# Optimization experiments

Hardware: AMD Instinct MI355X
Metric: run time of the kernel (lower is better)

## Reference

```python
import jax, jax.numpy as jnp
import numpy as np

EPS = 1e-9
NUM_HEADS = 16
D = 1024      # input_dim == hidden_dim
B, S = 2, 2048


def layer_norm(x, scale, shift):
    mu = x.mean(axis=-1, keepdims=True)
    # torch std is unbiased (ddof=1); eps added to std, not variance
    std = jnp.std(x, axis=-1, ddof=1, keepdims=True)
    return scale * (x - mu) / (std + EPS) + shift


def setup_inputs() -> dict:
    key = jax.random.key(0)
    ks = jax.random.split(key, 18)
    d, h = D, D
    w = lambda k, sh: jax.random.normal(k, sh, dtype=jnp.float32) * 0.02
    return {
        "inputs": jax.random.normal(ks[0], (B, S, d), dtype=jnp.float32),
        "ln1_scale": jax.random.normal(ks[1], (d,), dtype=jnp.float32),
        "ln1_shift": jax.random.normal(ks[2], (d,), dtype=jnp.float32),
        "Wq": w(ks[3], (d, h)), "bq": jnp.zeros((h,), jnp.float32),
        "Wk": w(ks[4], (d, h)), "bk": jnp.zeros((h,), jnp.float32),
        "Wv": w(ks[5], (d, h)), "bv": jnp.zeros((h,), jnp.float32),
        "Wo": w(ks[6], (h, d)), "bo": jnp.zeros((d,), jnp.float32),
        "W1": w(ks[7], (d, 4 * d)), "b1": jnp.zeros((4 * d,), jnp.float32),
        "W2": w(ks[8], (4 * d, d)), "b2": jnp.zeros((d,), jnp.float32),
        "ln2_scale": jax.random.normal(ks[9], (d,), dtype=jnp.float32),
        "ln2_shift": jax.random.normal(ks[10], (d,), dtype=jnp.float32),
    }


def mhsa(x, Wq, bq, Wk, bk, Wv, bv, Wo, bo):
    b, s, d = x.shape
    nh, dh = NUM_HEADS, D // NUM_HEADS
    q = (x @ Wq + bq).reshape(b, s, nh, dh).transpose(0, 2, 1, 3)  # b h s d
    k = (x @ Wk + bk).reshape(b, s, nh, dh).transpose(0, 2, 1, 3)
    v = (x @ Wv + bv).reshape(b, s, nh, dh).transpose(0, 2, 1, 3)
    scores = jnp.einsum("bhqd,bhkd->bhqk", q, k) / jnp.sqrt(jnp.float32(dh))
    causal = jnp.triu(jnp.ones((s, s), dtype=bool), k=1)  # mask above diagonal
    scores = jnp.where(causal, -jnp.inf, scores)
    p = jax.nn.softmax(scores, axis=-1)
    p = jnp.where(jnp.isnan(p), 0.0, p)  # NaN-fill as in original
    out = jnp.einsum("bhqk,bhkd->bhqd", p, v)
    out = out.transpose(0, 2, 1, 3).reshape(b, s, nh * dh)
    return out @ Wo + bo


def reference(inputs, ln1_scale, ln1_shift, Wq, bq, Wk, bk, Wv, bv, Wo, bo,
              W1, b1, W2, b2, ln2_scale, ln2_shift):
    o1 = layer_norm(inputs, ln1_scale, ln1_shift)
    o1 = mhsa(o1, Wq, bq, Wk, bk, Wv, bv, Wo, bo) + inputs
    o2 = layer_norm(o1, ln2_scale, ln2_shift)
    # NOTE: original adds the residual from the *normalized* tensor, not o1
    ffn = jax.nn.relu(o2 @ W1 + b1) @ W2 + b2
    return ffn + o2
```

## Files before the change

### kernel.cpp

```cpp
#include <hip/hip_runtime.h>
#include <hip/hip_bf16.h>
#include <math.h>

#define BB 2
#define SS 2048
#define DD 1024
#define HH 16
#define DH 64
#define NROW (BB*SS)
#define FFN (4*DD)

typedef __attribute__((ext_vector_type(8))) __bf16 bf16x8;
typedef __attribute__((ext_vector_type(4))) float f32x4;

__device__ __forceinline__ ushort f2b(float f) {
    union { float f; uint32_t u; } x; x.f = f;
    uint32_t r = x.u + 0x7FFF + ((x.u >> 16) & 1);
    return (ushort)(r >> 16);
}
__device__ __forceinline__ float b2f(ushort u) {
    union { uint32_t u; float f; } x; x.u = (uint32_t)u << 16;
    return x.f;
}

__global__ __launch_bounds__(256)
void ln_kernel(const float* __restrict__ x, const float* __restrict__ scale,
               const float* __restrict__ shift, ushort* __restrict__ y) {
    int row = blockIdx.x;
    const float* xr = x + (size_t)row * DD;
    ushort* yr = y + (size_t)row * DD;
    int t = threadIdx.x;
    float v[4];
    float s = 0.f, ss = 0.f;
#pragma unroll
    for (int i = 0; i < 4; ++i) {
        v[i] = xr[t + 256 * i];
        s += v[i];
        ss += v[i] * v[i];
    }
#pragma unroll
    for (int off = 32; off; off >>= 1) {
        s  += __shfl_xor(s, off);
        ss += __shfl_xor(ss, off);
    }
    __shared__ float red[8];
    int w = t >> 6;
    if ((t & 63) == 0) { red[w] = s; red[w + 4] = ss; }
    __syncthreads();
    float st  = red[0] + red[1] + red[2] + red[3];
    float sst = red[4] + red[5] + red[6] + red[7];
    float mu = st * (1.f / DD);
    float var = (sst - DD * mu * mu) * (1.f / (DD - 1));
    var = fmaxf(var, 0.f);
    float inv = 1.f / (sqrtf(var) + 1e-9f);
#pragma unroll
    for (int i = 0; i < 4; ++i) {
        int c = t + 256 * i;
        yr[c] = f2b(scale[c] * (v[i] - mu) * inv + shift[c]);
    }
}

__global__ __launch_bounds__(256)
void ln_res_kernel(const ushort* __restrict__ xa, const float* __restrict__ xb,
                   const float* __restrict__ scale, const float* __restrict__ shift,
                   ushort* __restrict__ yb) {
    int row = blockIdx.x;
    const ushort* ar = xa + (size_t)row * DD;
    const float* br = xb + (size_t)row * DD;
    ushort* ybr = yb + (size_t)row * DD;
    int t = threadIdx.x;
    float v[4];
    float s = 0.f, ss = 0.f;
#pragma unroll
    for (int i = 0; i < 4; ++i) {
        int c = t + 256 * i;
        v[i] = b2f(ar[c]) + br[c];
        s += v[i];
        ss += v[i] * v[i];
    }
#pragma unroll
    for (int off = 32; off; off >>= 1) {
        s  += __shfl_xor(s, off);
        ss += __shfl_xor(ss, off);
    }
    __shared__ float red[8];
    int w = t >> 6;
    if ((t & 63) == 0) { red[w] = s; red[w + 4] = ss; }
    __syncthreads();
    float st  = red[0] + red[1] + red[2] + red[3];
    float sst = red[4] + red[5] + red[6] + red[7];
    float mu = st * (1.f / DD);
    float var = (sst - DD * mu * mu) * (1.f / (DD - 1));
    var = fmaxf(var, 0.f);
    float inv = 1.f / (sqrtf(var) + 1e-9f);
#pragma unroll
    for (int i = 0; i < 4; ++i) {
        int c = t + 256 * i;
        ybr[c] = f2b(scale[c] * (v[i] - mu) * inv + shift[c]);
    }
}

__global__ __launch_bounds__(256)
void transpose_bf16_kernel(const float* __restrict__ W, ushort* __restrict__ Wt,
                           int K, int N) {
    __shared__ ushort tile[32][33];
    int tx = threadIdx.x & 31;
    int ty = threadIdx.x >> 5;
    int n0 = blockIdx.x * 32;
    int k0 = blockIdx.y * 32;
#pragma unroll
    for (int i = 0; i < 32; i += 8)
        tile[ty + i][tx] = f2b(W[(size_t)(k0 + ty + i) * N + n0 + tx]);
    __syncthreads();
#pragma unroll
    for (int i = 0; i < 32; i += 8)
        Wt[(size_t)(n0 + ty + i) * K + k0 + tx] = tile[tx][ty + i];
}

__global__ __launch_bounds__(256)
void reduce_wo_kernel(const float* __restrict__ p0, const float* __restrict__ p1,
                      const float* __restrict__ bias, ushort* __restrict__ yb) {
    int i = (blockIdx.x * 256 + threadIdx.x) * 4;
    float4 a = *reinterpret_cast<const float4*>(p0 + i);
    float4 b = *reinterpret_cast<const float4*>(p1 + i);
    int c = i & (DD - 1);
    float4 bs = *reinterpret_cast<const float4*>(bias + c);
    ushort4 o;
    o.x = f2b(a.x + b.x + bs.x);
    o.y = f2b(a.y + b.y + bs.y);
    o.z = f2b(a.z + b.z + bs.z);
    o.w = f2b(a.w + b.w + bs.w);
    *reinterpret_cast<ushort4*>(yb + i) = o;
}

__global__ __launch_bounds__(256)
void reduce_ffn2_kernel(const float* __restrict__ p0, const float* __restrict__ p1,
                        const float* __restrict__ bias, const ushort* __restrict__ res,
                        float* __restrict__ out) {
    int i = (blockIdx.x * 256 + threadIdx.x) * 4;
    float4 a = *reinterpret_cast<const float4*>(p0 + i);
    float4 b = *reinterpret_cast<const float4*>(p1 + i);
    ushort4 r = *reinterpret_cast<const ushort4*>(res + i);
    int c = i & (DD - 1);
    float4 bs = *reinterpret_cast<const float4*>(bias + c);
    float4 o;
    o.x = a.x + b.x + bs.x + b2f(r.x);
    o.y = a.y + b.y + bs.y + b2f(r.y);
    o.z = a.z + b.z + bs.z + b2f(r.z);
    o.w = a.w + b.w + bs.w + b2f(r.w);
    *reinterpret_cast<float4*>(out + i) = o;
}

#define GBM 128
#define GBN 128
#define GBK 32

template <int MODE, bool BF16_OUT, int DEPTH>
__global__ __launch_bounds__(512)
void gemm_bf16_kernel(const ushort* __restrict__ A, const ushort* __restrict__ Wt,
                      const float* __restrict__ bias, const ushort* __restrict__ addsrc,
                      void* __restrict__ Cout, int M, int N, int K, int lda,
                      const float* __restrict__ bias2, const float* __restrict__ bias3,
                      void* __restrict__ out2, void* __restrict__ out3) {
    __shared__ ushort As[DEPTH][GBM * GBK];
    __shared__ ushort Bs[DEPTH][GBN * GBK];

    int tid = threadIdx.x;
    int lane = tid & 63;
    int wid = tid >> 6;
    int wr = wid >> 2, wc = wid & 3;

    int gx = gridDim.x;
    int nwg = gx * gridDim.y;
    int orig = blockIdx.y * gx + blockIdx.x;
    int q8 = nwg >> 3;
    int swz = (orig & 7) * q8 + (orig >> 3);
    int bx = swz % gx, by = swz / gx;

    int brow = by * GBM;
    int bcol = bx * GBN;
    size_t koff = (size_t)blockIdx.z * K;

    int lrow = lane & 15;
    int kgrp = lane >> 4;

    f32x4 acc[4][2] = {};

    int srow = tid >> 2;
    int sgran = (tid & 3) ^ ((srow >> 1) & 3);

    auto stage = [&](int buf, int k0) {
        const char* ga = (const char*)A +
            ((size_t)(brow + srow) * lda + koff + k0) * 2 + sgran * 16;
        __builtin_amdgcn_global_load_lds(
            (const __attribute__((address_space(1))) uint32_t*)ga,
            (__attribute__((address_space(3))) uint32_t*)(&As[buf][0] + (wid * 16) * GBK),
            16, 0, 0);
        const char* gb = (const char*)Wt +
            ((size_t)(bcol + srow) * lda + koff + k0) * 2 + sgran * 16;
        __builtin_amdgcn_global_load_lds(
            (const __attribute__((address_space(1))) uint32_t*)gb,
            (__attribute__((address_space(3))) uint32_t*)(&Bs[buf][0] + (wid * 16) * GBK),
            16, 0, 0);
    };

    int nk = K / GBK;
    constexpr int PRE = DEPTH - 1;
#pragma unroll
    for (int s = 0; s < PRE; ++s)
        if (s < nk) stage(s, s * GBK);

    int cur = 0, stg = PRE;
    for (int t = 0; t < nk; ++t) {
        __builtin_amdgcn_sched_barrier(0);
        int rem = nk - 1 - t;
        if constexpr (DEPTH == 5) {
            if (rem >= 3)      asm volatile("s_waitcnt vmcnt(6)" ::: "memory");
            else if (rem == 2) asm volatile("s_waitcnt vmcnt(4)" ::: "memory");
            else if (rem == 1) asm volatile("s_waitcnt vmcnt(2)" ::: "memory");
            else               asm volatile("s_waitcnt vmcnt(0)" ::: "memory");
        } else {
            if (rem >= 1)      asm volatile("s_waitcnt vmcnt(2)" ::: "memory");
            else               asm volatile("s_waitcnt vmcnt(0)" ::: "memory");
        }
        asm volatile("s_barrier" ::: "memory");
        if (t + PRE < nk) stage(stg, (t + PRE) * GBK);

        bf16x8 afrag[4], bfrag[2];
#pragma unroll
        for (int mi = 0; mi < 4; ++mi) {
            int row = wr * 64 + mi * 16 + lrow;
            int gran = kgrp ^ ((row >> 1) & 3);
            afrag[mi] = *(const bf16x8*)((const char*)&As[cur][0] + row * 64 + gran * 16);
        }
#pragma unroll
        for (int ni = 0; ni < 2; ++ni) {
            int row = wc * 32 + ni * 16 + lrow;
            int gran = kgrp ^ ((row >> 1) & 3);
            bfrag[ni] = *(const bf16x8*)((const char*)&Bs[cur][0] + row * 64 + gran * 16);
        }
#pragma unroll
        for (int mi = 0; mi < 4; ++mi)
#pragma unroll
            for (int ni = 0; ni < 2; ++ni)
                acc[mi][ni] = __builtin_amdgcn_mfma_f32_16x16x32_bf16(
                    afrag[mi], bfrag[ni], acc[mi][ni], 0, 0, 0);

        cur = (cur == DEPTH - 1) ? 0 : cur + 1;
        stg = (stg == DEPTH - 1) ? 0 : stg + 1;
    }

    if (MODE == 3) {
        int which = bcol >> 10;
        const float* bs = which == 0 ? bias : (which == 1 ? bias2 : bias3);
#pragma unroll
        for (int ni = 0; ni < 2; ++ni) {
            int col = bcol + wc * 32 + ni * 16 + lrow;
            int lcol = col & 1023;
            float bsv = bs[lcol];
#pragma unroll
            for (int mi = 0; mi < 4; ++mi) {
                f32x4 a = acc[mi][ni];
#pragma unroll
                for (int j = 0; j < 4; ++j) {
                    int row = brow + wr * 64 + mi * 16 + kgrp * 4 + j;
                    float val = a[j] + bsv;
                    if (which == 2) {
                        size_t idx = (size_t)(row >> 11) * ((size_t)DD * SS)
                                   + (size_t)lcol * SS + (row & (SS - 1));
                        ((ushort*)out3)[idx] = f2b(val);
                    } else {
                        ushort* dst = which == 0 ? (ushort*)Cout : (ushort*)out2;
                        dst[(size_t)row * DD + lcol] = f2b(val);
                    }
                }
            }
        }
        return;
    }

    if (MODE == 4) {
        float* dst = (float*)Cout + (size_t)blockIdx.z * ((size_t)M * N);
#pragma unroll
        for (int ni = 0; ni < 2; ++ni) {
            int col = bcol + wc * 32 + ni * 16 + lrow;
#pragma unroll
            for (int mi = 0; mi < 4; ++mi) {
                f32x4 a = acc[mi][ni];
#pragma unroll
                for (int j = 0; j < 4; ++j) {
                    int row = brow + wr * 64 + mi * 16 + kgrp * 4 + j;
                    dst[(size_t)row * N + col] = a[j];
                }
            }
        }
        return;
    }

#pragma unroll
    for (int ni = 0; ni < 2; ++ni) {
        int col = bcol + wc * 32 + ni * 16 + lrow;
        float bsv = bias[col];
#pragma unroll
        for (int mi = 0; mi < 4; ++mi) {
            f32x4 a = acc[mi][ni];
#pragma unroll
            for (int j = 0; j < 4; ++j) {
                int row = brow + wr * 64 + mi * 16 + kgrp * 4 + j;
                float val = a[j] + bsv;
                if (MODE == 1) val = fmaxf(val, 0.f);
                if (BF16_OUT)
                    ((ushort*)Cout)[(size_t)row * N + col] = f2b(val);
                else
                    ((float*)Cout)[(size_t)row * N + col] = val;
            }
        }
    }
}

__global__ __launch_bounds__(256)
void attn_mfma_kernel(const ushort* __restrict__ Qg, const ushort* __restrict__ Kg,
                      const ushort* __restrict__ Vtg, ushort* __restrict__ Og) {
    __shared__ ushort Qs[64 * 64];
    __shared__ ushort Ks[2][64 * 64];
    __shared__ ushort Vs[2][64 * 64];

    int tid = threadIdx.x;
    int lane = tid & 63;
    int wid = tid >> 6;
    int bh = blockIdx.x;
    int b = bh >> 4, h = bh & 15;
    int q0 = ((int)gridDim.y - 1 - (int)blockIdx.y) * 64;

    const ushort* Qbase = Qg + ((size_t)(b * SS + q0)) * DD + h * DH;
    const ushort* Kbase = Kg + ((size_t)(b * SS)) * DD + h * DH;
    const ushort* Vbase = Vtg + (size_t)bh * DH * SS;

    int r0 = wid * 16;
    int rr0 = r0 + (lane >> 3);
    int g0 = lane & 7;
    int g = lane >> 4;
    int lr = lane & 15;

    auto stageKV = [&](int buf, int k0) {
#pragma unroll
        for (int i = 0; i < 2; ++i) {
            int rr = rr0 + i * 8;
            int gg = g0 ^ (rr & 7);
            const ushort* srck = Kbase + (size_t)(k0 + rr) * DD + gg * 8;
            __builtin_amdgcn_global_load_lds(
                (const __attribute__((address_space(1))) uint32_t*)srck,
                (__attribute__((address_space(3))) uint32_t*)(&Ks[buf][0] + (r0 + i * 8) * 64),
                16, 0, 0);
            const ushort* srcv = Vbase + (size_t)rr * SS + k0 + gg * 8;
            __builtin_amdgcn_global_load_lds(
                (const __attribute__((address_space(1))) uint32_t*)srcv,
                (__attribute__((address_space(3))) uint32_t*)(&Vs[buf][0] + (r0 + i * 8) * 64),
                16, 0, 0);
        }
    };

    int nt = q0 / 64 + 1;

    {
#pragma unroll
        for (int i = 0; i < 2; ++i) {
            int rr = rr0 + i * 8;
            int gg = g0 ^ (rr & 7);
            const ushort* src = Qbase + (size_t)rr * DD + gg * 8;
            __builtin_amdgcn_global_load_lds(
                (const __attribute__((address_space(1))) uint32_t*)src,
                (__attribute__((address_space(3))) uint32_t*)(Qs + (r0 + i * 8) * 64),
                16, 0, 0);
        }
    }
    stageKV(0, 0);
    asm volatile("s_waitcnt vmcnt(4)" ::: "memory");

    bf16x8 aq[2];
    {
        int r = wid * 16 + lr;
#pragma unroll
        for (int ks = 0; ks < 2; ++ks) {
            int lg = ks * 4 + g;
            aq[ks] = *(const bf16x8*)((const char*)Qs + r * 128 + ((lg ^ (r & 7)) << 4));
        }
    }
    ushort* Ps = Qs;

    f32x4 oacc[4] = {};
    float m = -INFINITY, l = 0.f;
    int qa = q0 + wid * 16 + lr;

    int cur = 0;
    for (int t = 0; t < nt; ++t) {
        __builtin_amdgcn_sched_barrier(0);
        asm volatile("s_waitcnt vmcnt(0)" ::: "memory");
        asm volatile("s_barrier" ::: "memory");
        if (t + 1 < nt) stageKV(cur ^ 1, (t + 1) * 64);
        int k0 = t * 64;

        f32x4 sacc[4] = {};
        __builtin_amdgcn_s_setprio(1);
#pragma unroll
        for (int ni = 0; ni < 4; ++ni) {
            int r = ni * 16 + lr;
#pragma unroll
            for (int ks = 0; ks < 2; ++ks) {
                int lg = ks * 4 + g;
                bf16x8 bk = *(const bf16x8*)((const char*)&Ks[cur][0] + r * 128 + ((lg ^ (r & 7)) << 4));
                sacc[ni] = __builtin_amdgcn_mfma_f32_16x16x32_bf16(bk, aq[ks], sacc[ni], 0, 0, 0);
            }
        }
        __builtin_amdgcn_s_setprio(0);

        float sc[4][4];
#pragma unroll
        for (int ni = 0; ni < 4; ++ni)
#pragma unroll
            for (int j = 0; j < 4; ++j)
                sc[ni][j] = sacc[ni][j] * 0.125f;
        if (k0 == q0) {
#pragma unroll
            for (int ni = 0; ni < 4; ++ni) {
#pragma unroll
                for (int j = 0; j < 4; ++j) {
                    int key = q0 + ni * 16 + g * 4 + j;
                    if (key > qa) sc[ni][j] = -INFINITY;
                }
            }
        }

        float mx = sc[0][0];
#pragma unroll
        for (int ni = 0; ni < 4; ++ni)
#pragma unroll
            for (int j = 0; j < 4; ++j) mx = fmaxf(mx, sc[ni][j]);
        mx = fmaxf(mx, __shfl_xor(mx, 16));
        mx = fmaxf(mx, __shfl_xor(mx, 32));
        float mn = fmaxf(m, mx);
        float corr = __expf(m - mn);
        m = mn;
        float p[4][4];
        float rs = 0.f;
#pragma unroll
        for (int ni = 0; ni < 4; ++ni)
#pragma unroll
            for (int j = 0; j < 4; ++j) { p[ni][j] = __expf(sc[ni][j] - mn); rs += p[ni][j]; }
        rs += __shfl_xor(rs, 16);
        rs += __shfl_xor(rs, 32);
        l = l * corr + rs;

        float cj[4];
#pragma unroll
        for (int j = 0; j < 4; ++j)
            cj[j] = __shfl(corr, (lane & 48) | (g * 4 + j));
#pragma unroll
        for (int ni = 0; ni < 4; ++ni)
#pragma unroll
            for (int j = 0; j < 4; ++j) oacc[ni][j] *= cj[j];

        {
            int row = wid * 16 + lr;
#pragma unroll
            for (int ni = 0; ni < 4; ++ni) {
                ushort4 w4;
                w4.x = f2b(p[ni][0]); w4.y = f2b(p[ni][1]);
                w4.z = f2b(p[ni][2]); w4.w = f2b(p[ni][3]);
                int gran = (ni * 2 + (g >> 1)) ^ (row & 7);
                *(ushort4*)((char*)Ps + row * 128 + (gran << 4) + (g & 1) * 8) = w4;
            }
        }
        asm volatile("s_waitcnt lgkmcnt(0)" ::: "memory");

        bf16x8 ap[2];
        {
            int r = wid * 16 + lr;
#pragma unroll
            for (int ks = 0; ks < 2; ++ks) {
                int lg = ks * 4 + g;
                ap[ks] = *(const bf16x8*)((const char*)Ps + r * 128 + ((lg ^ (r & 7)) << 4));
            }
        }
        __builtin_amdgcn_s_setprio(1);
#pragma unroll
        for (int ni = 0; ni < 4; ++ni) {
            int r = ni * 16 + lr;
#pragma unroll
            for (int ks = 0; ks < 2; ++ks) {
                int lg = ks * 4 + g;
                bf16x8 bv = *(const bf16x8*)((const char*)&Vs[cur][0] + r * 128 + ((lg ^ (r & 7)) << 4));
                oacc[ni] = __builtin_amdgcn_mfma_f32_16x16x32_bf16(ap[ks], bv, oacc[ni], 0, 0, 0);
            }
        }
        __builtin_amdgcn_s_setprio(0);
        cur ^= 1;
    }

#pragma unroll
    for (int j = 0; j < 4; ++j) {
        float lj = __shfl(l, (lane & 48) | (g * 4 + j));
        float inv = 1.f / lj;
        int gr = q0 + wid * 16 + g * 4 + j;
#pragma unroll
        for (int ni = 0; ni < 4; ++ni) {
            int d = ni * 16 + lr;
            Og[((size_t)(b * SS + gr)) * DD + h * DH + d] = f2b(oacc[ni][j] * inv);
        }
    }
}

extern "C" void kernel_launch(void* const* d_in, const int* in_sizes, int n_in,
                              void* d_out, int out_size, void* d_ws, size_t ws_size,
                              hipStream_t stream) {
    const float* inputs    = (const float*)d_in[0];
    const float* ln1_scale = (const float*)d_in[1];
    const float* ln1_shift = (const float*)d_in[2];
    const float* Wq = (const float*)d_in[3];
    const float* bq = (const float*)d_in[4];
    const float* Wk = (const float*)d_in[5];
    const float* bk = (const float*)d_in[6];
    const float* Wv = (const float*)d_in[7];
    const float* bv = (const float*)d_in[8];
    const float* Wo = (const float*)d_in[9];
    const float* bo = (const float*)d_in[10];
    const float* W1 = (const float*)d_in[11];
    const float* b1 = (const float*)d_in[12];
    const float* W2 = (const float*)d_in[13];
    const float* b2 = (const float*)d_in[14];
    const float* ln2_scale = (const float*)d_in[15];
    const float* ln2_shift = (const float*)d_in[16];
    float* out = (float*)d_out;

    const size_t MB = 1024 * 1024;
    char* w = (char*)d_ws;
    ushort* q_b   = (ushort*)(w + 0 * MB);
    ushort* k_b   = (ushort*)(w + 8 * MB);
    ushort* vt_b  = (ushort*)(w + 16 * MB);
    ushort* att_b = (ushort*)(w + 24 * MB);
    float*  pw    = (float*)(w + 32 * MB);
    ushort* proj_b= (ushort*)(w + 0 * MB);
    ushort* o2_b  = (ushort*)(w + 8 * MB);
    float*  pf    = (float*)(w + 16 * MB);
    ushort* h1_b  = (ushort*)(w + 64 * MB);
    ushort* wq_t  = (ushort*)(w + 96 * MB);
    ushort* wk_t  = (ushort*)(w + 98 * MB);
    ushort* wv_t  = (ushort*)(w + 100 * MB);
    ushort* wo_t  = (ushort*)(w + 102 * MB);
    ushort* w1_t  = (ushort*)(w + 104 * MB);
    ushort* w2_t  = (ushort*)(w + 112 * MB);
    ushort* xn_b  = (ushort*)(w + 120 * MB);

    transpose_bf16_kernel<<<dim3(DD / 32, DD / 32), 256, 0, stream>>>(Wq, wq_t, DD, DD);
    transpose_bf16_kernel<<<dim3(DD / 32, DD / 32), 256, 0, stream>>>(Wk, wk_t, DD, DD);
    transpose_bf16_kernel<<<dim3(DD / 32, DD / 32), 256, 0, stream>>>(Wv, wv_t, DD, DD);
    transpose_bf16_kernel<<<dim3(DD / 32, DD / 32), 256, 0, stream>>>(Wo, wo_t, DD, DD);
    transpose_bf16_kernel<<<dim3(FFN / 32, DD / 32), 256, 0, stream>>>(W1, w1_t, DD, FFN);
    transpose_bf16_kernel<<<dim3(DD / 32, FFN / 32), 256, 0, stream>>>(W2, w2_t, FFN, DD);

    ln_kernel<<<NROW, 256, 0, stream>>>(inputs, ln1_scale, ln1_shift, xn_b);

    dim3 gqkv(3 * DD / GBN, NROW / GBM, 1);
    gemm_bf16_kernel<3, true, 3><<<gqkv, 512, 0, stream>>>(
        xn_b, wq_t, bq, nullptr, q_b, NROW, 3 * DD, DD, DD, bk, bv, k_b, vt_b);

    dim3 ga(BB * HH, SS / 64);
    attn_mfma_kernel<<<ga, 256, 0, stream>>>(q_b, k_b, vt_b, att_b);

    dim3 g1z(DD / GBN, NROW / GBM, 2);
    gemm_bf16_kernel<4, false, 5><<<g1z, 512, 0, stream>>>(
        att_b, wo_t, nullptr, nullptr, pw, NROW, DD, DD / 2, DD, nullptr, nullptr, nullptr, nullptr);
    reduce_wo_kernel<<<(NROW * DD / 4) / 256, 256, 0, stream>>>(
        pw, pw + (size_t)NROW * DD, bo, proj_b);

    ln_res_kernel<<<NROW, 256, 0, stream>>>(proj_b, inputs, ln2_scale, ln2_shift, o2_b);

    dim3 g2(FFN / GBN, NROW / GBM, 1);
    gemm_bf16_kernel<1, true, 3><<<g2, 512, 0, stream>>>(
        o2_b, w1_t, b1, nullptr, h1_b, NROW, FFN, DD, DD, nullptr, nullptr, nullptr, nullptr);

    gemm_bf16_kernel<4, false, 5><<<g1z, 512, 0, stream>>>(
        h1_b, w2_t, nullptr, nullptr, pf, NROW, DD, FFN / 2, FFN, nullptr, nullptr, nullptr, nullptr);
    reduce_ffn2_kernel<<<(NROW * DD / 4) / 256, 256, 0, stream>>>(
        pf, pf + (size_t)NROW * DD, b2, o2_b, out);
}
```

Baseline: 257.0 us.

## Fold softmax scale into Q, use exp2 with lazy rescaling and remapped tile order

Pre-multiplies Q by log2(e)/sqrt(dh) in the projection epilogue so attention can use native exp2 without a per-score multiply. Adds FA4-style lazy rescaling that skips the output correction unless the running max grows by more than a threshold, and switches P conversion to native bf16 casts. Also changes the query-tile order across blockIdx.y to a serpentine pattern instead of strict reverse. The lazy rescaling lets p values exceed 1, up to about 2^11, which raises bf16 rounding error and overflow risk. The new tile order may also hurt load balance across the causal triangle.

```diff
diff --git a/kernel.cpp b/kernel.cpp
--- a/kernel.cpp
+++ b/kernel.cpp
@@ -11,7 +11,10 @@
 #define FFN (4*DD)
 
 typedef __attribute__((ext_vector_type(8))) __bf16 bf16x8;
+typedef __attribute__((ext_vector_type(4))) __bf16 bf16x4;
 typedef __attribute__((ext_vector_type(4))) float f32x4;
+
+#define QSCALE 0.18033688011112042f
 
 __device__ __forceinline__ ushort f2b(float f) {
     union { float f; uint32_t u; } x; x.f = f;
@@ -269,9 +272,10 @@
                         size_t idx = (size_t)(row >> 11) * ((size_t)DD * SS)
                                    + (size_t)lcol * SS + (row & (SS - 1));
                         ((ushort*)out3)[idx] = f2b(val);
+                    } else if (which == 0) {
+                        ((ushort*)Cout)[(size_t)row * DD + lcol] = f2b(val * QSCALE);
                     } else {
-                        ushort* dst = which == 0 ? (ushort*)Cout : (ushort*)out2;
-                        dst[(size_t)row * DD + lcol] = f2b(val);
+                        ((ushort*)out2)[(size_t)row * DD + lcol] = f2b(val);
                     }
                 }
             }
@@ -330,7 +334,10 @@
     int wid = tid >> 6;
     int bh = blockIdx.x;
     int b = bh >> 4, h = bh & 15;
-    int q0 = ((int)gridDim.y - 1 - (int)blockIdx.y) * 64;
+    int y = blockIdx.y;
+    int jj = y >> 3, kk = y & 7;
+    int qt = jj * 8 + ((jj & 1) ? 7 - kk : kk);
+    int q0 = qt * 64;
 
     const ushort* Qbase = Qg + ((size_t)(b * SS + q0)) * DD + h * DH;
     const ushort* Kbase = Kg + ((size_t)(b * SS)) * DD + h * DH;
@@ -390,6 +397,7 @@
 
     f32x4 oacc[4] = {};
     float m = -INFINITY, l = 0.f;
+    const float THR = 11.0f;
     int qa = q0 + wid * 16 + lr;
 
     int cur = 0;
@@ -414,61 +422,61 @@
         }
         __builtin_amdgcn_s_setprio(0);
 
-        float sc[4][4];
-#pragma unroll
-        for (int ni = 0; ni < 4; ++ni)
-#pragma unroll
-            for (int j = 0; j < 4; ++j)
-                sc[ni][j] = sacc[ni][j] * 0.125f;
         if (k0 == q0) {
 #pragma unroll
             for (int ni = 0; ni < 4; ++ni) {
 #pragma unroll
                 for (int j = 0; j < 4; ++j) {
                     int key = q0 + ni * 16 + g * 4 + j;
-                    if (key > qa) sc[ni][j] = -INFINITY;
+                    if (key > qa) sacc[ni][j] = -INFINITY;
                 }
             }
         }
 
-        float mx = sc[0][0];
+        float mx = sacc[0][0];
 #pragma unroll
         for (int ni = 0; ni < 4; ++ni)
 #pragma unroll
-            for (int j = 0; j < 4; ++j) mx = fmaxf(mx, sc[ni][j]);
+            for (int j = 0; j < 4; ++j) mx = fmaxf(mx, sacc[ni][j]);
         mx = fmaxf(mx, __shfl_xor(mx, 16));
         mx = fmaxf(mx, __shfl_xor(mx, 32));
-        float mn = fmaxf(m, mx);
-        float corr = __expf(m - mn);
-        m = mn;
+
+        if (__any(mx > m + THR)) {
+            float mn = fmaxf(m, mx);
+            float corr = __builtin_amdgcn_exp2f(m - mn);
+            m = mn;
+            l *= corr;
+            float cj[4];
+#pragma unroll
+            for (int j = 0; j < 4; ++j)
+                cj[j] = __shfl(corr, (lane & 48) | (g * 4 + j));
+#pragma unroll
+            for (int ni = 0; ni < 4; ++ni)
+#pragma unroll
+                for (int j = 0; j < 4; ++j) oacc[ni][j] *= cj[j];
+        }
+
         float p[4][4];
         float rs = 0.f;
 #pragma unroll
         for (int ni = 0; ni < 4; ++ni)
 #pragma unroll
-            for (int j = 0; j < 4; ++j) { p[ni][j] = __expf(sc[ni][j] - mn); rs += p[ni][j]; }
+            for (int j = 0; j < 4; ++j) {
+                p[ni][j] = __builtin_amdgcn_exp2f(sacc[ni][j] - m);
+                rs += p[ni][j];
+            }
         rs += __shfl_xor(rs, 16);
         rs += __shfl_xor(rs, 32);
-        l = l * corr + rs;
-
-        float cj[4];
-#pragma unroll
-        for (int j = 0; j < 4; ++j)
-            cj[j] = __shfl(corr, (lane & 48) | (g * 4 + j));
-#pragma unroll
-        for (int ni = 0; ni < 4; ++ni)
-#pragma unroll
-            for (int j = 0; j < 4; ++j) oacc[ni][j] *= cj[j];
+        l += rs;
 
         {
             int row = wid * 16 + lr;
 #pragma unroll
             for (int ni = 0; ni < 4; ++ni) {
-                ushort4 w4;
-                w4.x = f2b(p[ni][0]); w4.y = f2b(p[ni][1]);
-                w4.z = f2b(p[ni][2]); w4.w = f2b(p[ni][3]);
+                bf16x4 w4 = { (__bf16)p[ni][0], (__bf16)p[ni][1],
+                              (__bf16)p[ni][2], (__bf16)p[ni][3] };
                 int gran = (ni * 2 + (g >> 1)) ^ (row & 7);
-                *(ushort4*)((char*)Ps + row * 128 + (gran << 4) + (g & 1) * 8) = w4;
+                *(bf16x4*)((char*)Ps + row * 128 + (gran << 4) + (g & 1) * 8) = w4;
             }
         }
         asm volatile("s_waitcnt lgkmcnt(0)" ::: "memory");
```

Measured after the change: 255.1 us. Within noise of the previous version (-0.8%).
